# Kernel tuning notes

Measured on AMD Instinct MI355X. Metric: run time of the kernel, lower is better.

Reference implementation:

```python
import jax, jax.numpy as jnp
import numpy as np
from jax.scipy.special import logsumexp

# Special-tag indices (module-level globals in the original repo)
PAD_IDX, SOS_IDX, EOS_IDX = 0, 1, 2
NEG = -10000.0


def setup_inputs() -> dict:
    L, B, T = 1024, 2048, 16
    key = jax.random.key(0)
    k1, k2, k3, k4 = jax.random.split(key, 4)
    h = jax.random.normal(k1, (L, B, T), dtype=jnp.float32)
    y0 = jax.random.randint(k2, (L + 1, B), 0, T)  # gold tag path, [L+1, B]
    # prefix-of-ones mask from random lengths in [L//2, L]
    lengths = jax.random.randint(k4, (B,), L // 2, L + 1)
    mask = (jnp.arange(L)[:, None] < lengths[None, :]).astype(jnp.float32)
    # transition matrix, init as in CRF.__init__
    trans = jax.random.normal(k3, (T, T), dtype=jnp.float32) * 0.01
    trans = (trans.at[SOS_IDX, :].set(NEG)
                  .at[:, EOS_IDX].set(NEG)
                  .at[:, PAD_IDX].set(NEG)
                  .at[PAD_IDX, :].set(NEG)
                  .at[PAD_IDX, EOS_IDX].set(0.0)
                  .at[PAD_IDX, PAD_IDX].set(0.0))
    return {"h": h, "y0": y0, "mask": mask, "trans": trans}


def _crf_loss(h, y0, mask, trans):
    L, B, T = h.shape
    # ---- score(h, y0, mask): note original uses _emit = 0 (emissions unused here)
    # S[b] = sum_t trans[y0[t+1,b], y0[t,b]] * mask[t,b]  for t in [0, L-2]
    S = jnp.sum(trans[y0[1:L], y0[: L - 1]] * mask[: L - 1], axis=0)  # [B]
    lengths = jnp.sum(mask, axis=0).astype(jnp.int32)                  # [B]
    last_tag = y0[lengths, jnp.arange(B)]                              # [B]
    S = S + trans[PAD_IDX, last_tag]

    # ---- partition(h, mask): forward algorithm over sigmoid(h)
    hs = jax.nn.sigmoid(h)
    Z0 = jnp.full((B, T), NEG, dtype=h.dtype).at[:, SOS_IDX].set(0.0)

    def step(Z, xm):
        _h, _m = xm                                   # [B,T], [B]
        # _Z[b,i] = logsumexp_j( Z[b,j] + _h[b,i] + trans[i,j] )
        _Z = logsumexp(Z[:, None, :] + _h[:, :, None] + trans[None, :, :], axis=2)
        Z = _Z * _m[:, None] + Z * (1.0 - _m[:, None])
        return Z, None

    Z, _ = jax.lax.scan(step, Z0, (hs, mask))
    Z = logsumexp(Z + trans[EOS_IDX], axis=1)         # [B]

    return jnp.mean(Z - S)


def reference(h, y0, mask, trans):
    return _crf_loss(h, y0, mask, trans)
```

## Files before the change

kernel.cpp:

```cpp
#include <hip/hip_runtime.h>


typedef unsigned int u32;
typedef float f32x4 __attribute__((ext_vector_type(4)));
typedef short s16x4 __attribute__((ext_vector_type(4)));
typedef unsigned int u32x2 __attribute__((ext_vector_type(2)));

#define LOG2E 1.4426950408889634f
#define LN2   0.6931471805599453f
#define Bsz   2048
#define Lsz   1024

#if __has_builtin(__builtin_amdgcn_exp2f)
__device__ __forceinline__ float exp2x(float x){ return __builtin_amdgcn_exp2f(x); }
#else
__device__ __forceinline__ float exp2x(float x){ return exp2f(x); }
#endif
#if __has_builtin(__builtin_amdgcn_logf)
__device__ __forceinline__ float log2x(float x){ return __builtin_amdgcn_logf(x); }
#else
__device__ __forceinline__ float log2x(float x){ return log2f(x); }
#endif
#if __has_builtin(__builtin_amdgcn_rcpf)
__device__ __forceinline__ float rcpx(float x){ return __builtin_amdgcn_rcpf(x); }
#else
__device__ __forceinline__ float rcpx(float x){ return 1.0f/x; }
#endif

__device__ __forceinline__ u32 cvtpk_bf16(float lo, float hi){
  u32 r;
  asm("v_cvt_pk_bf16_f32 %0, %1, %2" : "=v"(r) : "v"(lo), "v"(hi));
  return r;
}

__device__ __forceinline__ f32x4 mfma_16x16x16_bf16(s16x4 a, s16x4 b, f32x4 c){
  f32x4 d;
  asm volatile("s_nop 1\n\t"
      "v_mfma_f32_16x16x16_bf16 %0, %1, %2, %3\n\t"
      "s_nop 7\n\t"
      "s_nop 7"
      : "=&v"(d) : "v"(a), "v"(b), "v"(c));
  return d;
}

__global__ __launch_bounds__(256) void k_zero(float* lenw, float* Sw, float* out){
  int i = blockIdx.x*256 + threadIdx.x;
  if (i < Bsz) lenw[i] = 0.f;
  else if (i < 2*Bsz) Sw[i - Bsz] = 0.f;
  if (i == 0) out[0] = 0.f;
}

__global__ __launch_bounds__(256) void k_score(const int* __restrict__ y0,
    const float* __restrict__ mask, const float* __restrict__ trans,
    float* __restrict__ lenw, float* __restrict__ Sw){
  __shared__ float Tt[256];
  Tt[threadIdx.x] = trans[threadIdx.x];
  __syncthreads();
  int gid = blockIdx.x*256 + threadIdx.x;
  int b  = gid & (Bsz-1);
  int tc = gid >> 11;
  int t0 = tc * 32;
  float lacc = 0.f, sacc = 0.f;
  int yc = y0[t0*Bsz + b];
  #pragma unroll 4
  for (int t = t0; t < t0+32; ++t) {
    float m = mask[t*Bsz + b];
    int yn = y0[(t+1)*Bsz + b];
    lacc += m;
    if (t <= Lsz-2) sacc += m * Tt[yn*16 + yc];
    yc = yn;
  }
  atomicAdd(&lenw[b], lacc);
  atomicAdd(&Sw[b], sacc);
}

__global__ __launch_bounds__(256) void k_phase1(const float* __restrict__ h,
    const float* __restrict__ trans, const float* __restrict__ lenw,
    u32x2* __restrict__ Pout){
  int wid = blockIdx.x*4 + (threadIdx.x >> 6);
  int c   = wid >> 11;
  int b   = wid & (Bsz-1);
  int lane = threadIdx.x & 63;
  int cl  = lane & 15;
  int grp = lane >> 4;
  int len = (int)(lenw[b] + 0.5f);
  int t0  = c << 6;
  int active = len - t0;
  if (active <= 0) return;
  if (active > 64) active = 64;

  const float* tp = trans + cl*16 + grp*4;
  float E0 = exp2x(tp[0]*LOG2E) * 0.0625f;
  float E1 = exp2x(tp[1]*LOG2E) * 0.0625f;
  float E2 = exp2x(tp[2]*LOG2E) * 0.0625f;
  float E3 = exp2x(tp[3]*LOG2E) * 0.0625f;

  int k0 = grp*4;
  u32 bx = ((k0+0)==cl ? 0x3F80u : 0u) | (((k0+1)==cl ? 0x3F80u : 0u) << 16);
  u32 by = ((k0+2)==cl ? 0x3F80u : 0u) | (((k0+3)==cl ? 0x3F80u : 0u) << 16);

  f32x4 zero4 = {0.f, 0.f, 0.f, 0.f};
  const float* hp = h + (size_t)(t0+grp)*(Bsz*16) + b*16 + cl;
  int a_addr0 = (cl      ) << 2;
  int a_addr1 = (cl | 16 ) << 2;
  int a_addr2 = (cl | 32 ) << 2;
  int a_addr3 = (cl | 48 ) << 2;

  for (int r = 0; r < 16; ++r) {
    int sb = r*4;
    if (sb >= active) break;
    float hv = *hp; hp += 4*(Bsz*16);
    float sg = rcpx(1.f + exp2x(hv * (-LOG2E)));
    float gv = exp2x(sg * LOG2E);
    int gvi = __float_as_int(gv);
    #pragma unroll
    for (int q = 0; q < 4; ++q) {
      if (sb + q >= active) break;
      int aaddr = (q==0) ? a_addr0 : (q==1) ? a_addr1 : (q==2) ? a_addr2 : a_addr3;
      float gq = __int_as_float(__builtin_amdgcn_ds_bpermute(aaddr, gvi));
      union { u32 u[2]; s16x4 v; } A, Bf;
      A.u[0] = cvtpk_bf16(gq*E0, gq*E1);
      A.u[1] = cvtpk_bf16(gq*E2, gq*E3);
      Bf.u[0] = bx; Bf.u[1] = by;
      f32x4 d = mfma_16x16x16_bf16(A.v, Bf.v, zero4);
      bx = cvtpk_bf16(d.x, d.y);
      by = cvtpk_bf16(d.z, d.w);
    }
  }
  Pout[(size_t)(b*16 + c)*64 + lane] = (u32x2){bx, by};
}

__global__ __launch_bounds__(256) void k_phase2(const u32x2* __restrict__ P,
    const float* __restrict__ trans, const float* __restrict__ lenw,
    const float* __restrict__ Sw, const int* __restrict__ y0,
    float* __restrict__ out){
  __shared__ float red[4];
  int b = blockIdx.x*4 + (threadIdx.x >> 6);
  int lane = threadIdx.x & 63;
  int cl = lane & 15, grp = lane >> 4;
  int len = (int)(lenw[b] + 0.5f);
  float v = (cl == 1) ? 1.f : 0.f;
  float lsc = 0.f;
  int nch = (len + 63) >> 6;
  const u32x2* Pb = P + (size_t)b*16*64;
  int srcaddr = (cl >> 2) << 6;
  int msel = cl & 3;
  for (int c = 0; c < nch; ++c) {
    u32x2 pw = Pb[c*64 + lane];
    float p0 = __uint_as_float(pw.x << 16);
    float p1 = __uint_as_float(pw.x & 0xffff0000u);
    float p2 = __uint_as_float(pw.y << 16);
    float p3 = __uint_as_float(pw.y & 0xffff0000u);
    float q0 = p0*v, q1 = p1*v, q2 = p2*v, q3 = p3*v;
    #pragma unroll
    for (int mk = 1; mk <= 8; mk <<= 1) {
      q0 += __shfl_xor(q0, mk);
      q1 += __shfl_xor(q1, mk);
      q2 += __shfl_xor(q2, mk);
      q3 += __shfl_xor(q3, mk);
    }
    float t0v = __int_as_float(__builtin_amdgcn_ds_bpermute(srcaddr, __float_as_int(q0)));
    float t1v = __int_as_float(__builtin_amdgcn_ds_bpermute(srcaddr, __float_as_int(q1)));
    float t2v = __int_as_float(__builtin_amdgcn_ds_bpermute(srcaddr, __float_as_int(q2)));
    float t3v = __int_as_float(__builtin_amdgcn_ds_bpermute(srcaddr, __float_as_int(q3)));
    float vn = (msel==0) ? t0v : (msel==1) ? t1v : (msel==2) ? t2v : t3v;
    float gm = fmaxf(fmaxf(q0,q1), fmaxf(q2,q3));
    gm = fmaxf(gm, __shfl_xor(gm, 16));
    gm = fmaxf(gm, __shfl_xor(gm, 32));
    int eb = (int)((__float_as_uint(gm) >> 23) & 0xff) - 127;
    float sc = __uint_as_float((u32)(127 - eb) << 23);
    v = vn * sc;
    lsc += (float)eb;
  }
  float eE = exp2x(trans[32 + cl] * LOG2E);
  float num = v * eE;
  num += __shfl_xor(num, 1);
  num += __shfl_xor(num, 2);
  num += __shfl_xor(num, 4);
  num += __shfl_xor(num, 8);
  if (lane == 0) {
    float Z = (log2x(num) + lsc + 4.f*(float)len) * LN2;
    int lastTag = y0[(size_t)len*Bsz + b];
    float Sb = Sw[b] + trans[lastTag];
    red[threadIdx.x >> 6] = (Z - Sb) * (1.f/(float)Bsz);
  }
  __syncthreads();
  if (threadIdx.x == 0) {
    atomicAdd(out, red[0] + red[1] + red[2] + red[3]);
  }
}

extern "C" void kernel_launch(void* const* d_in, const int* in_sizes, int n_in,
                              void* d_out, int out_size, void* d_ws, size_t ws_size,
                              hipStream_t stream) {
  const float* h     = (const float*)d_in[0];
  const int*   y0    = (const int*)d_in[1];
  const float* mask  = (const float*)d_in[2];
  const float* trans = (const float*)d_in[3];
  float* out  = (float*)d_out;
  float* lenw = (float*)d_ws;
  float* Sw   = lenw + Bsz;
  u32x2* P    = (u32x2*)((char*)d_ws + 16384);

  k_zero  <<<16,   256, 0, stream>>>(lenw, Sw, out);
  k_score <<<256,  256, 0, stream>>>(y0, mask, trans, lenw, Sw);
  k_phase1<<<8192, 256, 0, stream>>>(h, trans, lenw, P);
  k_phase2<<<512,  256, 0, stream>>>(P, trans, lenw, Sw, y0, out);
}
```

Baseline: 90.52 us.

## Interleave four chunk chains per wave and precompute sigmoid-exp into LDS

Phase 1 now assigns one block per batch element, and each wave processes four 64-step chunks at once. All sigmoid/exp values are first computed with coalesced loads and stored as bf16 in shared memory. The main loop then issues four independent MFMAs back-to-back, so the dependent-chain latency and the s_nop padding are amortised across four chains. The bpermute broadcasts and per-step global loads are gone. The cost is extra LDS use, more registers, and a tail path that handles partial chunks, with waves running full-length loops regardless of how active each chunk is.

```diff
diff --git a/kernel.cpp b/kernel.cpp
--- a/kernel.cpp
+++ b/kernel.cpp
@@ -10,6 +10,7 @@
 #define LN2   0.6931471805599453f
 #define Bsz   2048
 #define Lsz   1024
+#define BT    32768
 
 #if __has_builtin(__builtin_amdgcn_exp2f)
 __device__ __forceinline__ float exp2x(float x){ return __builtin_amdgcn_exp2f(x); }
@@ -33,7 +34,7 @@
   return r;
 }
 
-__device__ __forceinline__ f32x4 mfma_16x16x16_bf16(s16x4 a, s16x4 b, f32x4 c){
+__device__ __forceinline__ f32x4 mfma16(s16x4 a, s16x4 b, f32x4 c){
   f32x4 d;
   asm volatile("s_nop 1\n\t"
       "v_mfma_f32_16x16x16_bf16 %0, %1, %2, %3\n\t"
@@ -41,6 +42,23 @@
       "s_nop 7"
       : "=&v"(d) : "v"(a), "v"(b), "v"(c));
   return d;
+}
+
+__device__ __forceinline__ void mfma16x4(
+    s16x4 a0, s16x4 a1, s16x4 a2, s16x4 a3,
+    s16x4 b0, s16x4 b1, s16x4 b2, s16x4 b3,
+    f32x4 z, f32x4& d0, f32x4& d1, f32x4& d2, f32x4& d3){
+  asm volatile(
+      "s_nop 1\n\t"
+      "v_mfma_f32_16x16x16_bf16 %0, %4, %8, %12\n\t"
+      "v_mfma_f32_16x16x16_bf16 %1, %5, %9, %12\n\t"
+      "v_mfma_f32_16x16x16_bf16 %2, %6, %10, %12\n\t"
+      "v_mfma_f32_16x16x16_bf16 %3, %7, %11, %12\n\t"
+      "s_nop 7\n\t"
+      "s_nop 7"
+      : "=&v"(d0), "=&v"(d1), "=&v"(d2), "=&v"(d3)
+      : "v"(a0), "v"(a1), "v"(a2), "v"(a3),
+        "v"(b0), "v"(b1), "v"(b2), "v"(b3), "v"(z));
 }
 
 __global__ __launch_bounds__(256) void k_zero(float* lenw, float* Sw, float* out){
@@ -77,17 +95,37 @@
 __global__ __launch_bounds__(256) void k_phase1(const float* __restrict__ h,
     const float* __restrict__ trans, const float* __restrict__ lenw,
     u32x2* __restrict__ Pout){
-  int wid = blockIdx.x*4 + (threadIdx.x >> 6);
-  int c   = wid >> 11;
-  int b   = wid & (Bsz-1);
+  __shared__ u32 gbuf[16][16][34];
+  int warp = threadIdx.x >> 6;
+  int b    = blockIdx.x;
   int lane = threadIdx.x & 63;
-  int cl  = lane & 15;
-  int grp = lane >> 4;
-  int len = (int)(lenw[b] + 0.5f);
-  int t0  = c << 6;
-  int active = len - t0;
-  if (active <= 0) return;
-  if (active > 64) active = 64;
+  int cl   = lane & 15;
+  int grp  = lane >> 4;
+  int len  = (int)(lenw[b] + 0.5f);
+
+  int active[4], qc[4], tl[4];
+  #pragma unroll
+  for (int i = 0; i < 4; ++i) {
+    int a = len - ((warp + 4*i) << 6);
+    a = a < 0 ? 0 : (a > 64 ? 64 : a);
+    active[i] = a; qc[i] = a >> 2; tl[i] = a & 3;
+  }
+
+  #pragma unroll
+  for (int i = 0; i < 4; ++i) {
+    int t0 = (warp + 4*i) << 6;
+    const float* hp = h + (size_t)t0*BT + b*16 + cl;
+    u32* wrow = &gbuf[warp*4 + i][cl][0];
+    #pragma unroll
+    for (int u = 0; u < 8; ++u) {
+      int tt = 8*u + 2*grp;
+      float h0 = hp[(size_t)tt*BT];
+      float h1 = hp[(size_t)(tt+1)*BT];
+      float g0 = exp2x(rcpx(1.f + exp2x(h0 * (-LOG2E))) * LOG2E);
+      float g1 = exp2x(rcpx(1.f + exp2x(h1 * (-LOG2E))) * LOG2E);
+      wrow[4*u + grp] = cvtpk_bf16(g0, g1);
+    }
+  }
 
   const float* tp = trans + cl*16 + grp*4;
   float E0 = exp2x(tp[0]*LOG2E) * 0.0625f;
@@ -96,38 +134,80 @@
   float E3 = exp2x(tp[3]*LOG2E) * 0.0625f;
 
   int k0 = grp*4;
-  u32 bx = ((k0+0)==cl ? 0x3F80u : 0u) | (((k0+1)==cl ? 0x3F80u : 0u) << 16);
-  u32 by = ((k0+2)==cl ? 0x3F80u : 0u) | (((k0+3)==cl ? 0x3F80u : 0u) << 16);
-
-  f32x4 zero4 = {0.f, 0.f, 0.f, 0.f};
-  const float* hp = h + (size_t)(t0+grp)*(Bsz*16) + b*16 + cl;
-  int a_addr0 = (cl      ) << 2;
-  int a_addr1 = (cl | 16 ) << 2;
-  int a_addr2 = (cl | 32 ) << 2;
-  int a_addr3 = (cl | 48 ) << 2;
+  u32 ibx = ((k0+0)==cl ? 0x3F80u : 0u) | (((k0+1)==cl ? 0x3F80u : 0u) << 16);
+  u32 iby = ((k0+2)==cl ? 0x3F80u : 0u) | (((k0+3)==cl ? 0x3F80u : 0u) << 16);
+  u32 bx0=ibx, bx1=ibx, bx2=ibx, bx3=ibx;
+  u32 by0=iby, by1=iby, by2=iby, by3=iby;
+  u32 sx0=ibx, sx1=ibx, sx2=ibx, sx3=ibx;
+  u32 sy0=iby, sy1=iby, sy2=iby, sy3=iby;
+  const f32x4 z4 = {0.f, 0.f, 0.f, 0.f};
+
+  const u32* r0 = &gbuf[warp*4 + 0][cl][0];
+  const u32* r1 = &gbuf[warp*4 + 1][cl][0];
+  const u32* r2 = &gbuf[warp*4 + 2][cl][0];
+  const u32* r3 = &gbuf[warp*4 + 3][cl][0];
 
   for (int r = 0; r < 16; ++r) {
-    int sb = r*4;
-    if (sb >= active) break;
-    float hv = *hp; hp += 4*(Bsz*16);
-    float sg = rcpx(1.f + exp2x(hv * (-LOG2E)));
-    float gv = exp2x(sg * LOG2E);
-    int gvi = __float_as_int(gv);
+    u32x2 gp0 = *(const u32x2*)(r0 + 2*r);
+    u32x2 gp1 = *(const u32x2*)(r1 + 2*r);
+    u32x2 gp2 = *(const u32x2*)(r2 + 2*r);
+    u32x2 gp3 = *(const u32x2*)(r3 + 2*r);
     #pragma unroll
     for (int q = 0; q < 4; ++q) {
-      if (sb + q >= active) break;
-      int aaddr = (q==0) ? a_addr0 : (q==1) ? a_addr1 : (q==2) ? a_addr2 : a_addr3;
-      float gq = __int_as_float(__builtin_amdgcn_ds_bpermute(aaddr, gvi));
-      union { u32 u[2]; s16x4 v; } A, Bf;
-      A.u[0] = cvtpk_bf16(gq*E0, gq*E1);
-      A.u[1] = cvtpk_bf16(gq*E2, gq*E3);
-      Bf.u[0] = bx; Bf.u[1] = by;
-      f32x4 d = mfma_16x16x16_bf16(A.v, Bf.v, zero4);
-      bx = cvtpk_bf16(d.x, d.y);
-      by = cvtpk_bf16(d.z, d.w);
-    }
-  }
-  Pout[(size_t)(b*16 + c)*64 + lane] = (u32x2){bx, by};
+      u32 w0 = (q < 2) ? gp0.x : gp0.y;
+      u32 w1 = (q < 2) ? gp1.x : gp1.y;
+      u32 w2 = (q < 2) ? gp2.x : gp2.y;
+      u32 w3 = (q < 2) ? gp3.x : gp3.y;
+      float g0 = __uint_as_float((q & 1) ? (w0 & 0xffff0000u) : (w0 << 16));
+      float g1 = __uint_as_float((q & 1) ? (w1 & 0xffff0000u) : (w1 << 16));
+      float g2 = __uint_as_float((q & 1) ? (w2 & 0xffff0000u) : (w2 << 16));
+      float g3 = __uint_as_float((q & 1) ? (w3 & 0xffff0000u) : (w3 << 16));
+      union { u32 u[2]; s16x4 v; } A0,A1,A2,A3, B0,B1,B2,B3;
+      A0.u[0]=cvtpk_bf16(g0*E0,g0*E1); A0.u[1]=cvtpk_bf16(g0*E2,g0*E3);
+      A1.u[0]=cvtpk_bf16(g1*E0,g1*E1); A1.u[1]=cvtpk_bf16(g1*E2,g1*E3);
+      A2.u[0]=cvtpk_bf16(g2*E0,g2*E1); A2.u[1]=cvtpk_bf16(g2*E2,g2*E3);
+      A3.u[0]=cvtpk_bf16(g3*E0,g3*E1); A3.u[1]=cvtpk_bf16(g3*E2,g3*E3);
+      B0.u[0]=bx0; B0.u[1]=by0;  B1.u[0]=bx1; B1.u[1]=by1;
+      B2.u[0]=bx2; B2.u[1]=by2;  B3.u[0]=bx3; B3.u[1]=by3;
+      f32x4 d0,d1,d2,d3;
+      mfma16x4(A0.v,A1.v,A2.v,A3.v, B0.v,B1.v,B2.v,B3.v, z4, d0,d1,d2,d3);
+      bx0=cvtpk_bf16(d0.x,d0.y); by0=cvtpk_bf16(d0.z,d0.w);
+      bx1=cvtpk_bf16(d1.x,d1.y); by1=cvtpk_bf16(d1.z,d1.w);
+      bx2=cvtpk_bf16(d2.x,d2.y); by2=cvtpk_bf16(d2.z,d2.w);
+      bx3=cvtpk_bf16(d3.x,d3.y); by3=cvtpk_bf16(d3.z,d3.w);
+    }
+    if (r+1 == qc[0]) { sx0=bx0; sy0=by0; }
+    if (r+1 == qc[1]) { sx1=bx1; sy1=by1; }
+    if (r+1 == qc[2]) { sx2=bx2; sy2=by2; }
+    if (r+1 == qc[3]) { sx3=bx3; sy3=by3; }
+  }
+
+  u32 txa[4] = {sx0,sx1,sx2,sx3};
+  u32 tya[4] = {sy0,sy1,sy2,sy3};
+  const u32* rr[4] = {r0,r1,r2,r3};
+  #pragma unroll
+  for (int i = 0; i < 4; ++i) {
+    u32 tbx = txa[i], tby = tya[i];
+    if (tl[i] > 0) {
+      u32x2 gp = *(const u32x2*)(rr[i] + 2*qc[i]);
+      float ga = __uint_as_float(gp.x << 16);
+      float gb = __uint_as_float(gp.x & 0xffff0000u);
+      float gc = __uint_as_float(gp.y << 16);
+      float gs[3] = {ga, gb, gc};
+      for (int j = 0; j < tl[i]; ++j) {
+        float g = gs[j];
+        union { u32 u[2]; s16x4 v; } A, Bf;
+        A.u[0] = cvtpk_bf16(g*E0, g*E1);
+        A.u[1] = cvtpk_bf16(g*E2, g*E3);
+        Bf.u[0] = tbx; Bf.u[1] = tby;
+        f32x4 d = mfma16(A.v, Bf.v, z4);
+        tbx = cvtpk_bf16(d.x, d.y);
+        tby = cvtpk_bf16(d.z, d.w);
+      }
+    }
+    if (active[i] > 0)
+      Pout[(size_t)(b*16 + warp + 4*i)*64 + lane] = (u32x2){tbx, tby};
+  }
 }
 
 __global__ __launch_bounds__(256) void k_phase2(const u32x2* __restrict__ P,
@@ -204,6 +284,6 @@
 
   k_zero  <<<16,   256, 0, stream>>>(lenw, Sw, out);
   k_score <<<256,  256, 0, stream>>>(y0, mask, trans, lenw, Sw);
-  k_phase1<<<8192, 256, 0, stream>>>(h, trans, lenw, P);
+  k_phase1<<<2048, 256, 0, stream>>>(h, trans, lenw, P);
   k_phase2<<<512,  256, 0, stream>>>(P, trans, lenw, Sw, y0, out);
 }
```

Measured after the change: 102.8 us. +13.5%, slower.
